# Performance work log

Hardware: AMD Instinct MI355X
Metric: run time of the kernel (lower is better)

## Reference

```python
import jax, jax.numpy as jnp
import numpy as np

WS = 8          # window size (square)
GRID_H = 64     # patch grid height
GRID_W = 64     # patch grid width
B = 16          # batch
C = 256         # features per token
NH = 8          # heads
HD = C // NH    # head dim
NL = 2          # blocks in stage (plain + shifted)
N = WS * WS     # tokens per window
MLP_HID = 4 * C
CPB_HID = 512   # hidden width of continuous position-bias MLP


def _rel_index(ws):
    # standard swin relative position index, (N*N,) into (2ws-1)^2 table
    coords = np.stack(np.meshgrid(np.arange(ws), np.arange(ws), indexing='ij')).reshape(2, -1)
    rel = (coords[:, :, None] - coords[:, None, :]).transpose(1, 2, 0) + (ws - 1)  # (N,N,2)
    idx = rel[..., 0] * (2 * ws - 1) + rel[..., 1]
    return idx.reshape(-1).astype(np.int32)


def _rel_table(ws):
    # swinv2 log-spaced relative coords table, ((2ws-1)^2, 2)
    r = np.arange(-(ws - 1), ws, dtype=np.float32)
    tab = np.stack(np.meshgrid(r, r, indexing='ij'), -1)  # (2ws-1, 2ws-1, 2)
    tab = tab / (ws - 1) * 8.0  # pretrained_window_size=None -> normalize by window_size-1
    tab = np.sign(tab) * np.log2(np.abs(tab) + 1.0) / np.log2(8.0)
    return tab.reshape(-1, 2).astype(np.float32)


def _shift_mask(H, W, ws, shift):
    # (num_windows, N, N) additive mask with -100 between shifted regions
    img = np.zeros((H, W), np.int32)
    cnt = 0
    for hs in (slice(0, H - ws), slice(H - ws, H - shift), slice(H - shift, H)):
        for vs in (slice(0, W - ws), slice(W - ws, W - shift), slice(W - shift, W)):
            img[hs, vs] = cnt
            cnt += 1
    win = img.reshape(H // ws, ws, W // ws, ws).transpose(0, 2, 1, 3).reshape(-1, ws * ws)
    diff = win[:, None, :] != win[:, :, None]
    return np.where(diff, -100.0, 0.0).astype(np.float32)


REL_IDX = jnp.asarray(_rel_index(WS))
REL_TAB = jnp.asarray(_rel_table(WS))


def setup_inputs() -> dict:
    key = jax.random.key(0)
    ks = jax.random.split(key, 8)
    rn = lambda k, shape, s=0.02: jax.random.normal(k, shape, jnp.float32) * s
    return dict(
        tokens=jax.random.normal(ks[0], (B, GRID_H * GRID_W, C), jnp.float32),
        grid_h=GRID_H,
        grid_w=GRID_W,
        qkv_w=rn(ks[1], (NL, 3 * C, C)),
        qkv_b=jnp.zeros((NL, 3 * C), jnp.float32),
        logit_scale=jnp.full((NL, NH, 1, 1), np.log(10.0), jnp.float32),
        cpb_w1=rn(ks[2], (NL, CPB_HID, 2), 0.1),
        cpb_b1=jnp.zeros((NL, CPB_HID), jnp.float32),
        cpb_w2=rn(ks[3], (NL, NH, CPB_HID), 0.1),
        proj_w=rn(ks[4], (NL, C, C)),
        proj_b=jnp.zeros((NL, C), jnp.float32),
        norm1_s=jnp.ones((NL, C), jnp.float32),
        norm1_b=jnp.zeros((NL, C), jnp.float32),
        mlp_w1=rn(ks[5], (NL, MLP_HID, C)),
        mlp_b1=jnp.zeros((NL, MLP_HID), jnp.float32),
        mlp_w2=rn(ks[6], (NL, C, MLP_HID)),
        mlp_b2=jnp.zeros((NL, C), jnp.float32),
        norm2_s=jnp.ones((NL, C), jnp.float32),
        norm2_b=jnp.zeros((NL, C), jnp.float32),
    )


def _layernorm(x, s, b):
    m = jnp.mean(x, -1, keepdims=True)
    v = jnp.mean(jnp.square(x - m), -1, keepdims=True)
    return (x - m) * jax.lax.rsqrt(v + 1e-5) * s + b


def _window_attn(x, H, W, shift, qkv_w, qkv_b, logit_scale, cpb_w1, cpb_b1, cpb_w2, proj_w, proj_b):
    Bt = x.shape[0]
    x = x.reshape(Bt, H, W, C)
    if shift > 0:
        x = jnp.roll(x, (-shift, -shift), axis=(1, 2))
    nwh, nww = H // WS, W // WS
    # window partition: (Bt*nwh*nww, N, C)
    xw = x.reshape(Bt, nwh, WS, nww, WS, C).transpose(0, 1, 3, 2, 4, 5).reshape(-1, N, C)
    qkv = (xw @ qkv_w.T + qkv_b).reshape(-1, N, 3, NH, HD).transpose(2, 0, 3, 1, 4)
    q, k, v = qkv[0], qkv[1], qkv[2]  # (BW, NH, N, HD)
    # swinv2 scaled cosine attention
    q = q / (jnp.linalg.norm(q, axis=-1, keepdims=True) + 1e-12)
    k = k / (jnp.linalg.norm(k, axis=-1, keepdims=True) + 1e-12)
    scale = jnp.exp(jnp.minimum(logit_scale, jnp.log(100.0)))  # (NH,1,1)
    attn = jnp.einsum('bhnd,bhmd->bhnm', q, k) * scale
    # continuous relative position bias MLP
    cpb = jax.nn.relu(REL_TAB @ cpb_w1.T + cpb_b1) @ cpb_w2.T  # (M, NH)
    bias = 16.0 * jax.nn.sigmoid(cpb[REL_IDX].reshape(N, N, NH).transpose(2, 0, 1))
    attn = attn + bias
    if shift > 0:
        mask = jnp.asarray(_shift_mask(H, W, WS, shift))  # (nwin, N, N)
        nwin = mask.shape[0]
        attn = (attn.reshape(Bt, nwin, NH, N, N) + mask[None, :, None]).reshape(-1, NH, N, N)
    attn = jax.nn.softmax(attn, axis=-1)
    out = jnp.einsum('bhnm,bhmd->bhnd', attn, v).transpose(0, 2, 1, 3).reshape(-1, N, C)
    out = out @ proj_w.T + proj_b
    # window un-partition
    out = out.reshape(Bt, nwh, nww, WS, WS, C).transpose(0, 1, 3, 2, 4, 5).reshape(Bt, H, W, C)
    if shift > 0:
        out = jnp.roll(out, (shift, shift), axis=(1, 2))
    return out.reshape(Bt, H * W, C)


def reference(tokens, grid_h, grid_w, qkv_w, qkv_b, logit_scale, cpb_w1, cpb_b1, cpb_w2,
              proj_w, proj_b, norm1_s, norm1_b, mlp_w1, mlp_b1, mlp_w2, mlp_b2,
              norm2_s, norm2_b):
    x = tokens
    for i in range(NL):
        shift = 0 if i % 2 == 0 else WS // 2  # even blocks plain, odd blocks shifted
        a = _window_attn(x, grid_h, grid_w, shift, qkv_w[i], qkv_b[i], logit_scale[i],
                         cpb_w1[i], cpb_b1[i], cpb_w2[i], proj_w[i], proj_b[i])
        a = _layernorm(a, norm1_s[i], norm1_b[i])  # swinv2 post-norm
        x = x + a
        m = jax.nn.gelu(x @ mlp_w1[i].T + mlp_b1[i], approximate=False) @ mlp_w2[i].T + mlp_b2[i]
        m = _layernorm(m, norm2_s[i], norm2_b[i])
        x = x + m
    return x
```

## Files before the change

kernel.cpp:

```cpp
#include <hip/hip_runtime.h>
#include <math.h>

#define C_    256
#define NTOK  65536
#define HWIN  512

#define AP_LDS   (4*64*72*2 + 64*256*2)
#define MLP2_LDS ((2*64*64 + 2*4*64*64)*2)

typedef __bf16 bf16x8 __attribute__((ext_vector_type(8)));
typedef float  f32x4  __attribute__((ext_vector_type(4)));
#define MFMA16(a,b,c) __builtin_amdgcn_mfma_f32_16x16x32_bf16((a),(b),(c),0,0,0)

__device__ inline ushort f2b(float f) {
    unsigned u = __builtin_bit_cast(unsigned, f);
    return (ushort)((u + 0x7fffu + ((u >> 16) & 1u)) >> 16);
}

union BF8u { ushort u[8]; bf16x8 v; };
__device__ inline bf16x8 cvt8(float4 a, float4 b) {
    BF8u t;
    t.u[0] = f2b(a.x); t.u[1] = f2b(a.y); t.u[2] = f2b(a.z); t.u[3] = f2b(a.w);
    t.u[4] = f2b(b.x); t.u[5] = f2b(b.y); t.u[6] = f2b(b.z); t.u[7] = f2b(b.w);
    return t.v;
}

#define TILE_MFMA(ACC, A, B)                                   \
    _Pragma("unroll") for (int mf_ = 0; mf_ < 4; ++mf_)        \
        _Pragma("unroll") for (int nf_ = 0; nf_ < 4; ++nf_)    \
            ACC[mf_][nf_] = MFMA16(A[mf_], B[nf_], ACC[mf_][nf_]);

__global__ void f2b_kernel(ushort* __restrict__ dst, const float* __restrict__ src) {
    size_t i = ((size_t)blockIdx.x * 256 + threadIdx.x) * 4;
    float4 v = *reinterpret_cast<const float4*>(src + i);
    ushort4 u = { f2b(v.x), f2b(v.y), f2b(v.z), f2b(v.w) };
    *reinterpret_cast<ushort4*>(dst + i) = u;
}

__global__ void cpb_kernel(const float* __restrict__ w1, const float* __restrict__ b1,
                           const float* __restrict__ w2, float* __restrict__ biastab) {
    __shared__ float red[256];
    const int e = blockIdx.x;
    const int t = threadIdx.x;
    const int p = e / 15, q = e % 15;
    const float v0 = (float)(p - 7) * (8.0f / 7.0f);
    const float v1 = (float)(q - 7) * (8.0f / 7.0f);
    const float t0 = copysignf(log2f(fabsf(v0) + 1.0f) * (1.0f / 3.0f), v0);
    const float t1 = copysignf(log2f(fabsf(v1) + 1.0f) * (1.0f / 3.0f), v1);
    const float ha = fmaxf(0.0f, t0 * w1[t * 2]         + t1 * w1[t * 2 + 1]         + b1[t]);
    const float hb = fmaxf(0.0f, t0 * w1[(t + 256) * 2] + t1 * w1[(t + 256) * 2 + 1] + b1[t + 256]);
    for (int h = 0; h < 8; ++h) {
        __syncthreads();
        red[t] = ha * w2[h * 512 + t] + hb * w2[h * 512 + t + 256];
        __syncthreads();
        for (int s = 128; s > 0; s >>= 1) {
            if (t < s) red[t] += red[t + s];
            __syncthreads();
        }
        if (t == 0) biastab[e * 8 + h] = 16.0f / (1.0f + expf(-red[0]));
    }
}

__global__ void biasx_kernel(const float* __restrict__ biastab, float* __restrict__ biasx) {
    int h = blockIdx.x >> 6, n = blockIdx.x & 63, m = threadIdx.x;
    int idx = ((n >> 3) - (m >> 3) + 7) * 15 + ((n & 7) - (m & 7) + 7);
    biasx[((size_t)(h * 64 + n)) * 64 + m] = biastab[idx * 8 + h];
}

__global__ __launch_bounds__(256, 2) void qkv_kernel(
    const float* __restrict__ x, const ushort* __restrict__ qwb,
    const float* __restrict__ qb, ushort* __restrict__ q_ws,
    ushort* __restrict__ k_ws, ushort* __restrict__ vT_ws,
    int shift, int win0)
{
    __shared__ ushort xs[64 * 256];
    const int t = threadIdx.x;
    const int win = win0 + blockIdx.x, lwin = blockIdx.x;
    const int b = win >> 6, wh = (win >> 3) & 7, ww = win & 7;
    const int w = t >> 6, l = t & 63, lr = l & 15, lg = l >> 4;
    const int aswz = (lr & 7) << 3;
    const f32x4 zf = { 0.f, 0.f, 0.f, 0.f };

    {
        int row = t >> 2, seg = t & 3;
        int i = row >> 3, j = row & 7;
        int rr = (wh * 8 + i + shift) & 63;
        int cc = (ww * 8 + j + shift) & 63;
        const float* src = x + ((size_t)(b * 4096 + rr * 64 + cc)) * 256 + seg * 64;
        #pragma unroll
        for (int k8 = 0; k8 < 8; ++k8) {
            float4 v0 = *reinterpret_cast<const float4*>(src + k8 * 8);
            float4 v1 = *reinterpret_cast<const float4*>(src + k8 * 8 + 4);
            int col = seg * 64 + k8 * 8;
            *reinterpret_cast<bf16x8*>(xs + row * 256 + (col ^ ((row & 7) << 3))) = cvt8(v0, v1);
        }
    }
    __syncthreads();

#define QK_LA(D, KT) { int k0_ = (KT) * 32 + lg * 8;                                        \
    _Pragma("unroll") for (int mf_ = 0; mf_ < 4; ++mf_)                                     \
        D[mf_] = *reinterpret_cast<const bf16x8*>(xs + (mf_ * 16 + lr) * 256 + (k0_ ^ aswz)); }
#define QK_LB(D, KT) { int k0_ = (KT) * 32 + lg * 8;                                        \
    _Pragma("unroll") for (int nf_ = 0; nf_ < 4; ++nf_)                                     \
        D[nf_] = *reinterpret_cast<const bf16x8*>(qwb + (size_t)(colb + nf_ * 16 + lr) * 256 + k0_); }

    for (int round = 0; round < 3; ++round) {
        const int colb = round * 256 + w * 64;
        f32x4 acc[4][4];
        #pragma unroll
        for (int mf = 0; mf < 4; ++mf)
            #pragma unroll
            for (int nf = 0; nf < 4; ++nf) acc[mf][nf] = zf;

        bf16x8 pa0[4], pb0[4], pa1[4], pb1[4];
        QK_LA(pa0, 0); QK_LB(pb0, 0);
        #pragma unroll
        for (int kt = 0; kt < 8; kt += 2) {
            QK_LA(pa1, kt + 1); QK_LB(pb1, kt + 1);
            TILE_MFMA(acc, pa0, pb0);
            if (kt + 2 < 8) { QK_LA(pa0, kt + 2); QK_LB(pb0, kt + 2); }
            TILE_MFMA(acc, pa1, pb1);
        }

        #pragma unroll
        for (int nf = 0; nf < 4; ++nf) {
            float bb = qb[colb + nf * 16 + lr];
            #pragma unroll
            for (int mf = 0; mf < 4; ++mf)
                #pragma unroll
                for (int r = 0; r < 4; ++r) acc[mf][nf][r] += bb;
        }

        if (round < 2) {
            float ss0[4][4], ss1[4][4];
            #pragma unroll
            for (int mf = 0; mf < 4; ++mf)
                #pragma unroll
                for (int r = 0; r < 4; ++r) {
                    ss0[mf][r] = acc[mf][0][r] * acc[mf][0][r] + acc[mf][1][r] * acc[mf][1][r];
                    ss1[mf][r] = acc[mf][2][r] * acc[mf][2][r] + acc[mf][3][r] * acc[mf][3][r];
                }
            #pragma unroll
            for (int m = 1; m < 16; m <<= 1)
                #pragma unroll
                for (int mf = 0; mf < 4; ++mf)
                    #pragma unroll
                    for (int r = 0; r < 4; ++r) {
                        ss0[mf][r] += __shfl_xor(ss0[mf][r], m);
                        ss1[mf][r] += __shfl_xor(ss1[mf][r], m);
                    }
            ushort* dst = (round == 0) ? q_ws : k_ws;
            #pragma unroll
            for (int mf = 0; mf < 4; ++mf)
                #pragma unroll
                for (int r = 0; r < 4; ++r) {
                    float rs0 = 1.0f / (sqrtf(ss0[mf][r]) + 1e-12f);
                    float rs1 = 1.0f / (sqrtf(ss1[mf][r]) + 1e-12f);
                    size_t rowoff = ((size_t)lwin * 64 + mf * 16 + lg * 4 + r) * 256;
                    #pragma unroll
                    for (int nf = 0; nf < 4; ++nf)
                        dst[rowoff + w * 64 + nf * 16 + lr] =
                            f2b(acc[mf][nf][r] * (nf < 2 ? rs0 : rs1));
                }
        } else {
            #pragma unroll
            for (int nf = 0; nf < 4; ++nf) {
                int h = 2 * w + (nf >> 1);
                int chan = (nf & 1) * 16 + lr;
                ushort* vrow = vT_ws + (((size_t)lwin * 8 + h) * 32 + chan) * 64;
                #pragma unroll
                for (int mf = 0; mf < 4; ++mf)
                    #pragma unroll
                    for (int r = 0; r < 4; ++r)
                        vrow[mf * 16 + lg * 4 + r] = f2b(acc[mf][nf][r]);
            }
        }
    }
#undef QK_LA
#undef QK_LB
}

__global__ __launch_bounds__(256, 2) void attnproj_kernel(
    const ushort* __restrict__ q_ws, const ushort* __restrict__ k_ws,
    const ushort* __restrict__ vT_ws, const ushort* __restrict__ pwb,
    const float* __restrict__ pb, const float* __restrict__ lsc,
    const float* __restrict__ biasx, const float* __restrict__ n1s,
    const float* __restrict__ n1b, const float* __restrict__ xin,
    float* __restrict__ xout, int shift, int win0)
{
    extern __shared__ ushort sm[];
    ushort* aol  = sm + 4 * 64 * 72;
    float*  outT = (float*)sm;

    const int t = threadIdx.x;
    const int win = win0 + blockIdx.x, lwin = blockIdx.x;
    const int b = win >> 6, wh = (win >> 3) & 7, ww = win & 7;
    const int w = t >> 6, l = t & 63, lr = l & 15, lg = l >> 4;
    ushort* Pw = sm + w * 64 * 72;
    const size_t tokbase = (size_t)lwin * 64;
    const f32x4 zf = { 0.f, 0.f, 0.f, 0.f };

    int regc[4], regr[4][4];
    #pragma unroll
    for (int nf = 0; nf < 4; ++nf) {
        int kc = nf * 16 + lr;
        int pr = wh * 8 + (kc >> 3), pc = ww * 8 + (kc & 7);
        regc[nf] = ((pr < 56) ? 0 : ((pr < 60) ? 1 : 2)) * 3 +
                   ((pc < 56) ? 0 : ((pc < 60) ? 1 : 2));
    }
    #pragma unroll
    for (int mf = 0; mf < 4; ++mf)
        #pragma unroll
        for (int r = 0; r < 4; ++r) {
            int n = mf * 16 + lg * 4 + r;
            int pr = wh * 8 + (n >> 3), pc = ww * 8 + (n & 7);
            regr[mf][r] = ((pr < 56) ? 0 : ((pr < 60) ? 1 : 2)) * 3 +
                          ((pc < 56) ? 0 : ((pc < 60) ? 1 : 2));
        }

    for (int hr = 0; hr < 2; ++hr) {
        const int h = w * 2 + hr;

        f32x4 sacc[4][4];
        {
            bf16x8 aq[4], bk[4];
            #pragma unroll
            for (int mf = 0; mf < 4; ++mf)
                aq[mf] = *reinterpret_cast<const bf16x8*>(
                    q_ws + (tokbase + mf * 16 + lr) * 256 + h * 32 + lg * 8);
            #pragma unroll
            for (int nf = 0; nf < 4; ++nf)
                bk[nf] = *reinterpret_cast<const bf16x8*>(
                    k_ws + (tokbase + nf * 16 + lr) * 256 + h * 32 + lg * 8);
            #pragma unroll
            for (int mf = 0; mf < 4; ++mf)
                #pragma unroll
                for (int nf = 0; nf < 4; ++nf)
                    sacc[mf][nf] = MFMA16(aq[mf], bk[nf], zf);
        }

        const float scale = __expf(fminf(lsc[h], 4.6051702f));
        float mx[4][4], sum[4][4];
        #pragma unroll
        for (int mf = 0; mf < 4; ++mf)
            #pragma unroll
            for (int r = 0; r < 4; ++r) mx[mf][r] = -1e30f;

        #pragma unroll
        for (int nf = 0; nf < 4; ++nf)
            #pragma unroll
            for (int mf = 0; mf < 4; ++mf)
                #pragma unroll
                for (int r = 0; r < 4; ++r) {
                    float v = sacc[mf][nf][r] * scale +
                              biasx[((size_t)(h * 64 + mf * 16 + lg * 4 + r)) * 64 + nf * 16 + lr];
                    if (shift && regc[nf] != regr[mf][r]) v -= 100.0f;
                    sacc[mf][nf][r] = v;
                    mx[mf][r] = fmaxf(mx[mf][r], v);
                }
        #pragma unroll
        for (int m = 1; m < 16; m <<= 1)
            #pragma unroll
            for (int mf = 0; mf < 4; ++mf)
                #pragma unroll
                for (int r = 0; r < 4; ++r) mx[mf][r] = fmaxf(mx[mf][r], __shfl_xor(mx[mf][r], m));

        #pragma unroll
        for (int mf = 0; mf < 4; ++mf)
            #pragma unroll
            for (int r = 0; r < 4; ++r) sum[mf][r] = 0.f;
        #pragma unroll
        for (int nf = 0; nf < 4; ++nf)
            #pragma unroll
            for (int mf = 0; mf < 4; ++mf)
                #pragma unroll
                for (int r = 0; r < 4; ++r) {
                    float e = __expf(sacc[mf][nf][r] - mx[mf][r]);
                    sacc[mf][nf][r] = e;
                    sum[mf][r] += e;
                }
        #pragma unroll
        for (int m = 1; m < 16; m <<= 1)
            #pragma unroll
            for (int mf = 0; mf < 4; ++mf)
                #pragma unroll
                for (int r = 0; r < 4; ++r) sum[mf][r] += __shfl_xor(sum[mf][r], m);

        #pragma unroll
        for (int nf = 0; nf < 4; ++nf)
            #pragma unroll
            for (int mf = 0; mf < 4; ++mf)
                #pragma unroll
                for (int r = 0; r < 4; ++r)
                    Pw[(mf * 16 + lg * 4 + r) * 72 + nf * 16 + lr] = f2b(sacc[mf][nf][r]);

        f32x4 oacc[4][2];
        #pragma unroll
        for (int mf = 0; mf < 4; ++mf)
            #pragma unroll
            for (int nf = 0; nf < 2; ++nf) oacc[mf][nf] = zf;
        #pragma unroll
        for (int ks = 0; ks < 2; ++ks) {
            bf16x8 pa[4], bv[2];
            #pragma unroll
            for (int mf = 0; mf < 4; ++mf)
                pa[mf] = *reinterpret_cast<const bf16x8*>(Pw + (mf * 16 + lr) * 72 + ks * 32 + lg * 8);
            #pragma unroll
            for (int nf = 0; nf < 2; ++nf)
                bv[nf] = *reinterpret_cast<const bf16x8*>(
                    vT_ws + (((size_t)lwin * 8 + h) * 32 + nf * 16 + lr) * 64 + ks * 32 + lg * 8);
            #pragma unroll
            for (int mf = 0; mf < 4; ++mf)
                #pragma unroll
                for (int nf = 0; nf < 2; ++nf)
                    oacc[mf][nf] = MFMA16(pa[mf], bv[nf], oacc[mf][nf]);
        }

        #pragma unroll
        for (int mf = 0; mf < 4; ++mf)
            #pragma unroll
            for (int r = 0; r < 4; ++r) {
                float inv = 1.0f / sum[mf][r];
                int row = mf * 16 + lg * 4 + r;
                #pragma unroll
                for (int nf = 0; nf < 2; ++nf) {
                    int col = h * 32 + nf * 16 + lr;
                    aol[row * 256 + (col ^ ((row & 7) << 3))] = f2b(oacc[mf][nf][r] * inv);
                }
            }
    }
    __syncthreads();

    const int aswz = (lr & 7) << 3;
#define PJ_LA(D, KT) { int k0_ = (KT) * 32 + lg * 8;                                          \
    _Pragma("unroll") for (int mf_ = 0; mf_ < 4; ++mf_)                                       \
        D[mf_] = *reinterpret_cast<const bf16x8*>(aol + (mf_ * 16 + lr) * 256 + (k0_ ^ aswz)); }
#define PJ_LB(D, KT) { int k0_ = (KT) * 32 + lg * 8;                                          \
    _Pragma("unroll") for (int nf_ = 0; nf_ < 4; ++nf_)                                       \
        D[nf_] = *reinterpret_cast<const bf16x8*>(pwb + (size_t)(w * 64 + nf_ * 16 + lr) * 256 + k0_); }

    f32x4 acc[4][4];
    #pragma unroll
    for (int mf = 0; mf < 4; ++mf)
        #pragma unroll
        for (int nf = 0; nf < 4; ++nf) acc[mf][nf] = zf;
    {
        bf16x8 pa0[4], pb0[4], pa1[4], pb1[4];
        PJ_LA(pa0, 0); PJ_LB(pb0, 0);
        #pragma unroll
        for (int kt = 0; kt < 8; kt += 2) {
            PJ_LA(pa1, kt + 1); PJ_LB(pb1, kt + 1);
            TILE_MFMA(acc, pa0, pb0);
            if (kt + 2 < 8) { PJ_LA(pa0, kt + 2); PJ_LB(pb0, kt + 2); }
            TILE_MFMA(acc, pa1, pb1);
        }
    }
#undef PJ_LA
#undef PJ_LB
    __syncthreads();

    #pragma unroll
    for (int nf = 0; nf < 4; ++nf) {
        int c = w * 64 + nf * 16 + lr;
        float bb = pb[c];
        #pragma unroll
        for (int mf = 0; mf < 4; ++mf)
            #pragma unroll
            for (int r = 0; r < 4; ++r)
                outT[(mf * 16 + lg * 4 + r) * 264 + c] = acc[mf][nf][r] + bb;
    }
    __syncthreads();

    for (int u = 0; u < 16; ++u) {
        int tk = w * 16 + u;
        float v0 = outT[tk * 264 + l];
        float v1 = outT[tk * 264 + l + 64];
        float v2 = outT[tk * 264 + l + 128];
        float v3 = outT[tk * 264 + l + 192];
        float s = v0 + v1 + v2 + v3, ss = v0 * v0 + v1 * v1 + v2 * v2 + v3 * v3;
        for (int m = 1; m < 64; m <<= 1) { s += __shfl_xor(s, m); ss += __shfl_xor(ss, m); }
        float mean = s * (1.0f / 256.0f);
        float var  = ss * (1.0f / 256.0f) - mean * mean;
        float rs   = rsqrtf(var + 1e-5f);

        int i = tk >> 3, j = tk & 7;
        int pr = (wh * 8 + i + shift) & 63;
        int pc = (ww * 8 + j + shift) & 63;
        size_t gaddr = ((size_t)(b * 4096 + pr * 64 + pc)) * 256;
        xout[gaddr + l]       = xin[gaddr + l]       + (v0 - mean) * rs * n1s[l]       + n1b[l];
        xout[gaddr + l + 64]  = xin[gaddr + l + 64]  + (v1 - mean) * rs * n1s[l + 64]  + n1b[l + 64];
        xout[gaddr + l + 128] = xin[gaddr + l + 128] + (v2 - mean) * rs * n1s[l + 128] + n1b[l + 128];
        xout[gaddr + l + 192] = xin[gaddr + l + 192] + (v3 - mean) * rs * n1s[l + 192] + n1b[l + 192];
    }
}

__global__ __launch_bounds__(256, 2) void mlp1_kernel(
    const float* __restrict__ x, const ushort* __restrict__ w1b,
    const float* __restrict__ b1, ushort* __restrict__ hidb, int tok_base)
{
    __shared__ ushort xs[64 * 256];
    const int t = threadIdx.x;
    const size_t ltok0 = (size_t)blockIdx.x * 64;
    const size_t tok0  = (size_t)tok_base + ltok0;
    const int w = t >> 6, l = t & 63, lr = l & 15, lg = l >> 4;
    const int aswz = (lr & 7) << 3;
    const f32x4 zf = { 0.f, 0.f, 0.f, 0.f };

    {
        int row = t >> 2, seg = t & 3;
        const float* src = x + (tok0 + row) * 256 + seg * 64;
        #pragma unroll
        for (int k8 = 0; k8 < 8; ++k8) {
            float4 v0 = *reinterpret_cast<const float4*>(src + k8 * 8);
            float4 v1 = *reinterpret_cast<const float4*>(src + k8 * 8 + 4);
            int col = seg * 64 + k8 * 8;
            *reinterpret_cast<bf16x8*>(xs + row * 256 + (col ^ ((row & 7) << 3))) = cvt8(v0, v1);
        }
    }
    __syncthreads();

#define M1_LA(D, KT) { int k0_ = (KT) * 32 + lg * 8;                                        \
    _Pragma("unroll") for (int mf_ = 0; mf_ < 4; ++mf_)                                     \
        D[mf_] = *reinterpret_cast<const bf16x8*>(xs + (mf_ * 16 + lr) * 256 + (k0_ ^ aswz)); }
#define M1_LB(D, KT) { int k0_ = (KT) * 32 + lg * 8;                                        \
    _Pragma("unroll") for (int nf_ = 0; nf_ < 4; ++nf_)                                     \
        D[nf_] = *reinterpret_cast<const bf16x8*>(w1b + (size_t)(n0 + nf_ * 16 + lr) * 256 + k0_); }

    for (int q = 0; q < 4; ++q) {
        const int n0 = q * 256 + w * 64;
        f32x4 acc[4][4];
        #pragma unroll
        for (int mf = 0; mf < 4; ++mf)
            #pragma unroll
            for (int nf = 0; nf < 4; ++nf) acc[mf][nf] = zf;

        bf16x8 pa0[4], pb0[4], pa1[4], pb1[4];
        M1_LA(pa0, 0); M1_LB(pb0, 0);
        #pragma unroll
        for (int kt = 0; kt < 8; kt += 2) {
            M1_LA(pa1, kt + 1); M1_LB(pb1, kt + 1);
            TILE_MFMA(acc, pa0, pb0);
            if (kt + 2 < 8) { M1_LA(pa0, kt + 2); M1_LB(pb0, kt + 2); }
            TILE_MFMA(acc, pa1, pb1);
        }

        #pragma unroll
        for (int nf = 0; nf < 4; ++nf) {
            int hcol = n0 + nf * 16 + lr;
            float bb = b1[hcol];
            #pragma unroll
            for (int mf = 0; mf < 4; ++mf)
                #pragma unroll
                for (int r = 0; r < 4; ++r) {
                    float pre = acc[mf][nf][r] + bb;
                    float g = 0.5f * pre * (1.0f + erff(pre * 0.70710678f));
                    hidb[(ltok0 + mf * 16 + lg * 4 + r) * 1024 + hcol] = f2b(g);
                }
        }
    }
#undef M1_LA
#undef M1_LB
}

__global__ __launch_bounds__(256, 2) void mlp2_kernel(
    const ushort* __restrict__ hidb, const ushort* __restrict__ w2b,
    const float* __restrict__ b2, const float* __restrict__ n2s,
    const float* __restrict__ n2b, float* __restrict__ x, int tok_base)
{
    extern __shared__ ushort sm3[];
    ushort* As = sm3;
    ushort* Bs = sm3 + 2 * 64 * 64;
    float*  outT = (float*)sm3;

    const int t = threadIdx.x;
    const size_t ltok0 = (size_t)blockIdx.x * 64;
    const size_t tok0  = (size_t)tok_base + ltok0;
    const int w = t >> 6, l = t & 63, lr = l & 15, lg = l >> 4;
    const f32x4 zf = { 0.f, 0.f, 0.f, 0.f };

    const int arow = t >> 2, aslot0 = (t & 3) * 2;
    const ushort* agp = hidb + (ltok0 + arow) * 1024;
    const ushort* bgp = w2b + (size_t)(w * 64 + l) * 1024;

    bf16x8 areg[2], breg[8];
    #pragma unroll
    for (int i = 0; i < 2; ++i)
        areg[i] = *reinterpret_cast<const bf16x8*>(agp + (aslot0 + i) * 8);
    #pragma unroll
    for (int s = 0; s < 8; ++s)
        breg[s] = *reinterpret_cast<const bf16x8*>(bgp + s * 8);
    {
        ushort* aw = As + arow * 64;
        ushort* bw = Bs + (size_t)(w * 64 + l) * 64;
        #pragma unroll
        for (int i = 0; i < 2; ++i)
            *reinterpret_cast<bf16x8*>(aw + (((aslot0 + i) ^ (arow & 7)) * 8)) = areg[i];
        #pragma unroll
        for (int s = 0; s < 8; ++s)
            *reinterpret_cast<bf16x8*>(bw + ((s ^ (l & 7)) * 8)) = breg[s];
    }

    f32x4 acc[4][4];
    #pragma unroll
    for (int mf = 0; mf < 4; ++mf)
        #pragma unroll
        for (int nf = 0; nf < 4; ++nf) acc[mf][nf] = zf;

    for (int kt = 0; kt < 16; ++kt) {
        const int cur = kt & 1, nxt = cur ^ 1;
        if (kt + 1 < 16) {
            #pragma unroll
            for (int i = 0; i < 2; ++i)
                areg[i] = *reinterpret_cast<const bf16x8*>(agp + (kt + 1) * 64 + (aslot0 + i) * 8);
            #pragma unroll
            for (int s = 0; s < 8; ++s)
                breg[s] = *reinterpret_cast<const bf16x8*>(bgp + (kt + 1) * 64 + s * 8);
        }
        __syncthreads();

        const ushort* ar = As + cur * 64 * 64;
        const ushort* br = Bs + (size_t)(cur * 4 + w) * 64 * 64;
        #pragma unroll
        for (int k2 = 0; k2 < 2; ++k2) {
            bf16x8 a[4], b[4];
            #pragma unroll
            for (int mf = 0; mf < 4; ++mf)
                a[mf] = *reinterpret_cast<const bf16x8*>(
                    ar + (mf * 16 + lr) * 64 + (((k2 * 4 + lg) ^ (lr & 7)) * 8));
            #pragma unroll
            for (int nf = 0; nf < 4; ++nf)
                b[nf] = *reinterpret_cast<const bf16x8*>(
                    br + (nf * 16 + lr) * 64 + (((k2 * 4 + lg) ^ (lr & 7)) * 8));
            TILE_MFMA(acc, a, b);
        }
        __syncthreads();

        if (kt + 1 < 16) {
            ushort* aw = As + nxt * 64 * 64 + arow * 64;
            ushort* bw = Bs + (size_t)(nxt * 4 + w) * 64 * 64 + (size_t)l * 64;
            #pragma unroll
            for (int i = 0; i < 2; ++i)
                *reinterpret_cast<bf16x8*>(aw + (((aslot0 + i) ^ (arow & 7)) * 8)) = areg[i];
            #pragma unroll
            for (int s = 0; s < 8; ++s)
                *reinterpret_cast<bf16x8*>(bw + ((s ^ (l & 7)) * 8)) = breg[s];
        }
    }
    __syncthreads();

    #pragma unroll
    for (int nf = 0; nf < 4; ++nf) {
        int c = w * 64 + nf * 16 + lr;
        float bb = b2[c];
        #pragma unroll
        for (int mf = 0; mf < 4; ++mf)
            #pragma unroll
            for (int r = 0; r < 4; ++r)
                outT[(mf * 16 + lg * 4 + r) * 264 + c] = acc[mf][nf][r] + bb;
    }
    __syncthreads();

    for (int u = 0; u < 16; ++u) {
        int tk = w * 16 + u;
        float v0 = outT[tk * 264 + l];
        float v1 = outT[tk * 264 + l + 64];
        float v2 = outT[tk * 264 + l + 128];
        float v3 = outT[tk * 264 + l + 192];
        float s = v0 + v1 + v2 + v3, ss = v0 * v0 + v1 * v1 + v2 * v2 + v3 * v3;
        for (int m = 1; m < 64; m <<= 1) { s += __shfl_xor(s, m); ss += __shfl_xor(ss, m); }
        float mean = s * (1.0f / 256.0f);
        float var  = ss * (1.0f / 256.0f) - mean * mean;
        float rs   = rsqrtf(var + 1e-5f);
        float* xp = x + (tok0 + tk) * 256;
        xp[l]       += (v0 - mean) * rs * n2s[l]       + n2b[l];
        xp[l + 64]  += (v1 - mean) * rs * n2s[l + 64]  + n2b[l + 64];
        xp[l + 128] += (v2 - mean) * rs * n2s[l + 128] + n2b[l + 128];
        xp[l + 192] += (v3 - mean) * rs * n2s[l + 192] + n2b[l + 192];
    }
}

extern "C" void kernel_launch(void* const* d_in, const int* in_sizes, int n_in,
                              void* d_out, int out_size, void* d_ws, size_t ws_size,
                              hipStream_t stream) {
    (void)in_sizes; (void)n_in; (void)out_size;
    const float* tokens = (const float*)d_in[0];
    const float* qkv_w  = (const float*)d_in[3];
    const float* qkv_b  = (const float*)d_in[4];
    const float* lsc    = (const float*)d_in[5];
    const float* cw1    = (const float*)d_in[6];
    const float* cb1    = (const float*)d_in[7];
    const float* cw2    = (const float*)d_in[8];
    const float* pw     = (const float*)d_in[9];
    const float* pb     = (const float*)d_in[10];
    const float* n1s    = (const float*)d_in[11];
    const float* n1b    = (const float*)d_in[12];
    const float* mw1    = (const float*)d_in[13];
    const float* mb1    = (const float*)d_in[14];
    const float* mw2    = (const float*)d_in[15];
    const float* mb2    = (const float*)d_in[16];
    const float* n2s    = (const float*)d_in[17];
    const float* n2b    = (const float*)d_in[18];

    float* x = (float*)d_out;

    ushort* pwb   = (ushort*)d_ws;
    ushort* w1b   = pwb + 2 * 256 * 256;
    ushort* w2b   = w1b + 2 * 1024 * 256;
    ushort* qwb   = w2b + 2 * 256 * 1024;
    float*  biasx = (float*)(qwb + 2 * 768 * 256);
    float*  biastab = biasx + 8 * 64 * 64;
    char*   big   = (char*)d_ws + 3407872;

    ushort* q_ws  = (ushort*)big;
    ushort* k_ws  = q_ws + (size_t)HWIN * 64 * 256;
    ushort* vT_ws = k_ws + (size_t)HWIN * 64 * 256;
    ushort* hidb  = (ushort*)big;

    size_t avail = ws_size - 3407872;
    int chunk_tok = (avail >= (size_t)32768 * 2048) ? 32768 : 16384;

    f2b_kernel<<<dim3(2 * 256 * 256 / 1024),  dim3(256), 0, stream>>>(pwb, pw);
    f2b_kernel<<<dim3(2 * 1024 * 256 / 1024), dim3(256), 0, stream>>>(w1b, mw1);
    f2b_kernel<<<dim3(2 * 256 * 1024 / 1024), dim3(256), 0, stream>>>(w2b, mw2);
    f2b_kernel<<<dim3(2 * 768 * 256 / 1024),  dim3(256), 0, stream>>>(qwb, qkv_w);

    for (int l = 0; l < 2; ++l) {
        const int shift = l ? 4 : 0;
        const float* xsrc = (l == 0) ? tokens : x;
        cpb_kernel<<<dim3(225), dim3(256), 0, stream>>>(
            cw1 + (size_t)l * 1024, cb1 + (size_t)l * 512, cw2 + (size_t)l * 4096, biastab);
        biasx_kernel<<<dim3(512), dim3(64), 0, stream>>>(biastab, biasx);
        for (int half = 0; half < 2; ++half) {
            qkv_kernel<<<dim3(HWIN), dim3(256), 0, stream>>>(
                xsrc, qwb + (size_t)l * 196608, qkv_b + (size_t)l * 768,
                q_ws, k_ws, vT_ws, shift, half * HWIN);
            attnproj_kernel<<<dim3(HWIN), dim3(256), AP_LDS, stream>>>(
                q_ws, k_ws, vT_ws, pwb + (size_t)l * 65536, pb + (size_t)l * 256,
                lsc + (size_t)l * 8, biasx, n1s + (size_t)l * 256, n1b + (size_t)l * 256,
                xsrc, x, shift, half * HWIN);
        }
        for (int tb = 0; tb < NTOK; tb += chunk_tok) {
            mlp1_kernel<<<dim3(chunk_tok / 64), dim3(256), 0, stream>>>(
                x, w1b + (size_t)l * 262144, mb1 + (size_t)l * 1024, hidb, tb);
            mlp2_kernel<<<dim3(chunk_tok / 64), dim3(256), MLP2_LDS, stream>>>(
                hidb, w2b + (size_t)l * 262144, mb2 + (size_t)l * 256,
                n2s + (size_t)l * 256, n2b + (size_t)l * 256, x, tb);
        }
    }
}
```

Before: 795.4 us.

## Stage MLP1 output through LDS, use tanh-approx GELU, triple-buffer B fragments

In mlp1 the GELU outputs are written into an LDS staging tile and then stored to global memory as coalesced 16-byte vectors, replacing scattered 2-byte stores. The exact erf GELU is replaced with a sigmoid/tanh-style approximation built on exp and a fast reciprocal. The QKV and MLP1 GEMM inner loops now prefetch B fragments two steps ahead in a three-slot ring and load A fragments just in time. This adds 32KB of LDS and extra barriers, and the GELU approximation changes numerics slightly.

```diff
diff --git a/kernel.cpp b/kernel.cpp
--- a/kernel.cpp
+++ b/kernel.cpp
@@ -15,6 +15,11 @@
 __device__ inline ushort f2b(float f) {
     unsigned u = __builtin_bit_cast(unsigned, f);
     return (ushort)((u + 0x7fffu + ((u >> 16) & 1u)) >> 16);
+}
+
+__device__ inline float fast_gelu(float x) {
+    float u = 1.5957691216f * x + 0.0713548163f * x * x * x;
+    return x * __builtin_amdgcn_rcpf(1.0f + __expf(-u));
 }
 
 union BF8u { ushort u[8]; bf16x8 v; };
@@ -112,14 +117,14 @@
             #pragma unroll
             for (int nf = 0; nf < 4; ++nf) acc[mf][nf] = zf;
 
-        bf16x8 pa0[4], pb0[4], pa1[4], pb1[4];
-        QK_LA(pa0, 0); QK_LB(pb0, 0);
-        #pragma unroll
-        for (int kt = 0; kt < 8; kt += 2) {
-            QK_LA(pa1, kt + 1); QK_LB(pb1, kt + 1);
-            TILE_MFMA(acc, pa0, pb0);
-            if (kt + 2 < 8) { QK_LA(pa0, kt + 2); QK_LB(pb0, kt + 2); }
-            TILE_MFMA(acc, pa1, pb1);
+        bf16x8 pb[3][4];
+        QK_LB(pb[0], 0); QK_LB(pb[1], 1);
+        #pragma unroll
+        for (int kt = 0; kt < 8; ++kt) {
+            if (kt + 2 < 8) QK_LB(pb[(kt + 2) % 3], kt + 2);
+            bf16x8 pa[4];
+            QK_LA(pa, kt);
+            TILE_MFMA(acc, pa, pb[kt % 3]);
         }
 
         #pragma unroll
@@ -399,6 +404,7 @@
     const float* __restrict__ b1, ushort* __restrict__ hidb, int tok_base)
 {
     __shared__ ushort xs[64 * 256];
+    __shared__ ushort hstage[64 * 256];
     const int t = threadIdx.x;
     const size_t ltok0 = (size_t)blockIdx.x * 64;
     const size_t tok0  = (size_t)tok_base + ltok0;
@@ -434,28 +440,37 @@
             #pragma unroll
             for (int nf = 0; nf < 4; ++nf) acc[mf][nf] = zf;
 
-        bf16x8 pa0[4], pb0[4], pa1[4], pb1[4];
-        M1_LA(pa0, 0); M1_LB(pb0, 0);
-        #pragma unroll
-        for (int kt = 0; kt < 8; kt += 2) {
-            M1_LA(pa1, kt + 1); M1_LB(pb1, kt + 1);
-            TILE_MFMA(acc, pa0, pb0);
-            if (kt + 2 < 8) { M1_LA(pa0, kt + 2); M1_LB(pb0, kt + 2); }
-            TILE_MFMA(acc, pa1, pb1);
-        }
+        bf16x8 pb[3][4];
+        M1_LB(pb[0], 0); M1_LB(pb[1], 1);
+        #pragma unroll
+        for (int kt = 0; kt < 8; ++kt) {
+            if (kt + 2 < 8) M1_LB(pb[(kt + 2) % 3], kt + 2);
+            bf16x8 pa[4];
+            M1_LA(pa, kt);
+            TILE_MFMA(acc, pa, pb[kt % 3]);
+        }
+
+        if (q > 0) __syncthreads();
 
         #pragma unroll
         for (int nf = 0; nf < 4; ++nf) {
-            int hcol = n0 + nf * 16 + lr;
-            float bb = b1[hcol];
-            #pragma unroll
-            for (int mf = 0; mf < 4; ++mf)
-                #pragma unroll
-                for (int r = 0; r < 4; ++r) {
-                    float pre = acc[mf][nf][r] + bb;
-                    float g = 0.5f * pre * (1.0f + erff(pre * 0.70710678f));
-                    hidb[(ltok0 + mf * 16 + lg * 4 + r) * 1024 + hcol] = f2b(g);
-                }
+            int lcol = w * 64 + nf * 16 + lr;
+            float bb = b1[q * 256 + lcol];
+            #pragma unroll
+            for (int mf = 0; mf < 4; ++mf)
+                #pragma unroll
+                for (int r = 0; r < 4; ++r)
+                    hstage[(mf * 16 + lg * 4 + r) * 256 + lcol] =
+                        f2b(fast_gelu(acc[mf][nf][r] + bb));
+        }
+        __syncthreads();
+
+        #pragma unroll
+        for (int j = 0; j < 8; ++j) {
+            int c = j * 256 + t;
+            int row = c >> 5, cc = (c & 31) * 8;
+            *reinterpret_cast<bf16x8*>(hidb + (ltok0 + row) * 1024 + q * 256 + cc) =
+                *reinterpret_cast<const bf16x8*>(hstage + row * 256 + cc);
         }
     }
 #undef M1_LA
```

After: 742.5 us. -6.6%, faster.
